# Kernel tuning notes

Measured on AMD Instinct MI355X. Metric: run time of the kernel, lower is better.

Reference implementation:

```python
import jax, jax.numpy as jnp
import numpy as np

EMBED_DIM = 512
NUM_HEADS = 8
HEAD_DIM = EMBED_DIM // NUM_HEADS
FFN_DIM = 4 * EMBED_DIM
B, S = 4, 2048
LN_EPS = 1e-5


def _linear_params(key, fan_in, fan_out):
    kw, kb = jax.random.split(key)
    bound = 1.0 / np.sqrt(fan_in)
    W = jax.random.uniform(kw, (fan_in, fan_out), jnp.float32, -bound, bound)
    b = jax.random.uniform(kb, (fan_out,), jnp.float32, -bound, bound)
    return W, b


def setup_inputs() -> dict:
    key = jax.random.key(0)
    ks = jax.random.split(key, 10)
    query = jax.random.normal(ks[0], (B, S, EMBED_DIM), jnp.float32)
    key_t = jax.random.normal(ks[1], (B, S, EMBED_DIM), jnp.float32)
    value = jax.random.normal(ks[2], (B, S, EMBED_DIM), jnp.float32)
    Wq, bq = _linear_params(ks[3], EMBED_DIM, EMBED_DIM)
    Wk, bk = _linear_params(ks[4], EMBED_DIM, EMBED_DIM)
    Wv, bv = _linear_params(ks[5], EMBED_DIM, EMBED_DIM)
    Wo, bo = _linear_params(ks[6], EMBED_DIM, EMBED_DIM)
    W1, b1 = _linear_params(ks[7], EMBED_DIM, FFN_DIM)
    W2, b2 = _linear_params(ks[8], FFN_DIM, EMBED_DIM)
    g1 = jnp.ones((EMBED_DIM,), jnp.float32); be1 = jnp.zeros((EMBED_DIM,), jnp.float32)
    g2 = jnp.ones((EMBED_DIM,), jnp.float32); be2 = jnp.zeros((EMBED_DIM,), jnp.float32)
    return dict(query=query, key=key_t, value=value,
                Wq=Wq, bq=bq, Wk=Wk, bk=bk, Wv=Wv, bv=bv, Wo=Wo, bo=bo,
                g1=g1, be1=be1, g2=g2, be2=be2,
                W1=W1, b1=b1, W2=W2, b2=b2)


def _layernorm(x, g, b):
    mu = jnp.mean(x, axis=-1, keepdims=True)
    var = jnp.mean(jnp.square(x - mu), axis=-1, keepdims=True)
    return (x - mu) * jax.lax.rsqrt(var + LN_EPS) * g + b


def reference(query, key, value, Wq, bq, Wk, bk, Wv, bv, Wo, bo,
              g1, be1, g2, be2, W1, b1, W2, b2):
    b_, s_ = query.shape[:2]
    # projections -> [B, H, S, Dh]
    Q = (query @ Wq + bq).reshape(b_, -1, NUM_HEADS, HEAD_DIM).transpose(0, 2, 1, 3)
    K = (key @ Wk + bk).reshape(b_, -1, NUM_HEADS, HEAD_DIM).transpose(0, 2, 1, 3)
    V = (value @ Wv + bv).reshape(b_, -1, NUM_HEADS, HEAD_DIM).transpose(0, 2, 1, 3)
    scores = jnp.einsum('bhqd,bhkd->bhqk', Q, K) / jnp.sqrt(jnp.float32(HEAD_DIM))
    attn = jax.nn.softmax(scores, axis=-1)  # dropout is eval-mode identity
    ctx = jnp.einsum('bhqk,bhkd->bhqd', attn, V)
    ctx = ctx.transpose(0, 2, 1, 3).reshape(b_, -1, EMBED_DIM)
    out = ctx @ Wo + bo
    out = _layernorm(query + out, g1, be1)
    ffn = jax.nn.gelu(out @ W1 + b1, approximate=False) @ W2 + b2
    return _layernorm(out + ffn, g2, be2)
```

## Files before the change

### kernel.cpp

```cpp
#include <hip/hip_runtime.h>
#include <hip/hip_bf16.h>
#include <math.h>

#define EMBED 512
#define NHEAD 8
#define HDIM 64
#define FFN 2048
#define BB 4
#define SS 2048
#define MROWS (BB*SS)
#define NB ((size_t)MROWS * EMBED)
#define LN_EPS 1e-5f
#define QSCALE 0.180336880111f

typedef __attribute__((ext_vector_type(8))) short short8;
typedef __attribute__((ext_vector_type(4))) float floatx4;

__device__ inline float bf2f(__hip_bfloat16 x) { return __bfloat162float(x); }
__device__ inline __hip_bfloat16 f2bf(float x) { return __float2bfloat16(x); }

__device__ inline float gelu_f(float x) {
    return 0.5f * x * (1.0f + erff(x * 0.70710678118654752f));
}

__device__ inline void async_copy16(const void* g, void* l) {
    __builtin_amdgcn_global_load_lds(
        (const __attribute__((address_space(1))) void*)g,
        (__attribute__((address_space(3))) void*)l, 16, 0, 0);
}

__device__ inline int sane_f(float v) {
    return (v == v) && (fabsf(v) > 0x1p-40f) && (fabsf(v) < 0x1p40f);
}

__global__ void detect_kernel(const void* __restrict__ q, int* __restrict__ flag) {
    const float* qf = (const float*)q;
    int lane = threadIdx.x;
    float v = qf[lane * 1024 + 7];
    bool ok = sane_f(v);
    unsigned long long m = __ballot(ok);
    if (lane == 0) *flag = (__popcll(m) >= 32) ? 1 : 0;
}

__global__ __launch_bounds__(256) void prep_kernel(
    const void* __restrict__ query, const void* __restrict__ keyi, const void* __restrict__ vali,
    const void* __restrict__ Wq, const void* __restrict__ Wk, const void* __restrict__ Wv,
    const void* __restrict__ Wo, const void* __restrict__ W1, const void* __restrict__ W2,
    const void* __restrict__ bq, const void* __restrict__ bk, const void* __restrict__ bv,
    const void* __restrict__ bo, const void* __restrict__ b1, const void* __restrict__ b2,
    const void* __restrict__ g1, const void* __restrict__ be1,
    const void* __restrict__ g2, const void* __restrict__ be2,
    __hip_bfloat16* __restrict__ qkvbf,
    __hip_bfloat16* __restrict__ Wcat,
    __hip_bfloat16* __restrict__ biasb)
{
    __shared__ __hip_bfloat16 L[64][65];
    const int f32 = sane_f(((const float*)query)[7]) + sane_f(((const float*)query)[1031]) +
                    sane_f(((const float*)query)[200003]) + sane_f(((const float*)query)[1000003]) >= 3;
    const int t = threadIdx.x;
    const int blk = blockIdx.x;

    if (blk < 6144) {
        size_t pos = ((size_t)blk * 256 + t) * 8;
        int sel = (int)(pos >> 22);
        size_t off = pos & (NB - 1);
        const void* src = sel == 0 ? query : sel == 1 ? keyi : vali;
        if (f32) {
            const float* s = (const float*)src + off;
            float4 f0 = *reinterpret_cast<const float4*>(s);
            float4 f1 = *reinterpret_cast<const float4*>(s + 4);
            alignas(16) __hip_bfloat16 h[8] = {
                f2bf(f0.x), f2bf(f0.y), f2bf(f0.z), f2bf(f0.w),
                f2bf(f1.x), f2bf(f1.y), f2bf(f1.z), f2bf(f1.w)};
            *reinterpret_cast<uint4*>(qkvbf + pos) = *reinterpret_cast<const uint4*>(h);
        } else {
            *reinterpret_cast<uint4*>(qkvbf + pos) =
                *reinterpret_cast<const uint4*>((const __hip_bfloat16*)src + off);
        }
        return;
    }

    const void* src; __hip_bfloat16* dst; int R, C, r0, c0;
    if (blk < 6400) {
        int b2i = blk - 6144; src = W1; dst = Wcat + 4 * 512 * 512;
        R = 512; C = 2048; r0 = (b2i >> 5) * 64; c0 = (b2i & 31) * 64;
    } else if (blk < 6656) {
        int b3 = blk - 6400; src = W2; dst = Wcat + 4 * 512 * 512 + 512 * 2048;
        R = 2048; C = 512; r0 = (b3 >> 3) * 64; c0 = (b3 & 7) * 64;
    } else if (blk < 6912) {
        int b4 = blk - 6656; int which = b4 >> 6; int tile = b4 & 63;
        src = which == 0 ? Wq : which == 1 ? Wk : which == 2 ? Wv : Wo;
        dst = Wcat + (size_t)which * 512 * 512;
        R = 512; C = 512; r0 = (tile >> 3) * 64; c0 = (tile & 7) * 64;
    } else {
        const void* srcs[10] = {bq, bk, bv, bo, b1, b2, g1, be1, g2, be2};
        const int offs[10] = {0, 512, 1024, 1536, 2048, 4096, 4608, 5120, 5632, 6144};
        const int lens[10] = {512, 512, 512, 512, 2048, 512, 512, 512, 512, 512};
        for (int a = 0; a < 10; ++a)
            for (int i = t; i < lens[a]; i += 256)
                biasb[offs[a] + i] = f32 ? f2bf(((const float*)srcs[a])[i])
                                         : ((const __hip_bfloat16*)srcs[a])[i];
        return;
    }
    for (int c = t; c < 4096; c += 256) {
        int lr = c >> 6, lc = c & 63;
        L[lr][lc] = f32 ? f2bf(((const float*)src)[(size_t)(r0 + lr) * C + c0 + lc])
                        : ((const __hip_bfloat16*)src)[(size_t)(r0 + lr) * C + c0 + lc];
    }
    __syncthreads();
    for (int c = t; c < 4096; c += 256) {
        int lr = c >> 6, lc = c & 63;
        dst[(size_t)(c0 + lr) * R + r0 + lc] = L[lc][lr];
    }
}

template<int ACT, int BIAS>
__global__ __launch_bounds__(256) void gemm_bt_lds_kernel(
    const __hip_bfloat16* __restrict__ A,
    const __hip_bfloat16* __restrict__ Bt,
    const __hip_bfloat16* __restrict__ bias,
    __hip_bfloat16* __restrict__ C,
    int M, int N, int K, int ksplit)
{
    const int bm = blockIdx.x * 128;
    const int bn = blockIdx.y * 128;
    int kbeg = 0, kend = K;
    if (BIAS == 0) {
        kbeg = blockIdx.z * ksplit;
        kend = kbeg + ksplit;
        C += (size_t)blockIdx.z * NB;
    }
    const int t = threadIdx.x;
    const int wave = t >> 6, lane = t & 63;
    const int wm = (wave >> 1) * 64, wn = (wave & 1) * 64;
    const int quad = lane >> 4, r = lane & 15;

    __shared__ alignas(16) __hip_bfloat16 As[2][128 * 32];
    __shared__ alignas(16) __hip_bfloat16 Bs[2][128 * 32];

    floatx4 acc[4][4];
    #pragma unroll
    for (int i = 0; i < 4; ++i)
        #pragma unroll
        for (int j = 0; j < 4; ++j)
            acc[i][j] = (floatx4){0.f, 0.f, 0.f, 0.f};

    const int c0 = wave * 128;

    for (int kt = kbeg; kt < kend; kt += 64) {
        #pragma unroll
        for (int h = 0; h < 2; ++h) {
            #pragma unroll
            for (int it = 0; it < 2; ++it) {
                int c = c0 + it * 64 + lane;
                int row = c >> 2, col = (c & 3) * 8;
                async_copy16(A + (size_t)(bm + row) * K + kt + h * 32 + col,
                             As[h] + (size_t)(c0 + it * 64) * 8);
                async_copy16(Bt + (size_t)(bn + row) * K + kt + h * 32 + col,
                             Bs[h] + (size_t)(c0 + it * 64) * 8);
            }
        }
        __syncthreads();
        #pragma unroll
        for (int h = 0; h < 2; ++h) {
            short8 af[4], bfr[4];
            #pragma unroll
            for (int i = 0; i < 4; ++i)
                af[i] = *reinterpret_cast<const short8*>(&As[h][(wm + i * 16 + r) * 32 + quad * 8]);
            #pragma unroll
            for (int j = 0; j < 4; ++j)
                bfr[j] = *reinterpret_cast<const short8*>(&Bs[h][(wn + j * 16 + r) * 32 + quad * 8]);
            #pragma unroll
            for (int i = 0; i < 4; ++i)
                #pragma unroll
                for (int j = 0; j < 4; ++j)
                    acc[i][j] = __builtin_amdgcn_mfma_f32_16x16x32_bf16(af[i], bfr[j], acc[i][j], 0, 0, 0);
        }
        __syncthreads();
    }

    #pragma unroll
    for (int j = 0; j < 4; ++j) {
        const int n = bn + wn + j * 16 + r;
        float bvv = BIAS ? bf2f(bias[n]) : 0.f;
        #pragma unroll
        for (int i = 0; i < 4; ++i) {
            #pragma unroll
            for (int v = 0; v < 4; ++v) {
                int m = bm + wm + i * 16 + quad * 4 + v;
                float x = acc[i][j][v] + bvv;
                if (ACT == 1) x = gelu_f(x);
                C[(size_t)m * N + n] = f2bf(x);
            }
        }
    }
}

__global__ __launch_bounds__(256) void gemm_qkv_fused_kernel(
    const __hip_bfloat16* __restrict__ Acat,
    const __hip_bfloat16* __restrict__ Wcat,
    const __hip_bfloat16* __restrict__ biascat,
    __hip_bfloat16* __restrict__ Ocat)
{
    const int sel = blockIdx.x >> 6;
    const __hip_bfloat16* A = Acat + (size_t)sel * NB;
    const __hip_bfloat16* Bt = Wcat + (size_t)sel * 512 * 512;
    const __hip_bfloat16* bias = biascat + sel * 512;
    __hip_bfloat16* C = Ocat + (size_t)sel * NB;

    const int bm = (blockIdx.x & 63) * 128;
    const int bn = blockIdx.y * 128;
    const int t = threadIdx.x;
    const int wave = t >> 6, lane = t & 63;
    const int wm = (wave >> 1) * 64, wn = (wave & 1) * 64;
    const int quad = lane >> 4, r = lane & 15;
    const int K = EMBED, N = EMBED;

    __shared__ alignas(16) __hip_bfloat16 As[2][128 * 32];
    __shared__ alignas(16) __hip_bfloat16 Bs[2][128 * 32];

    floatx4 acc[4][4];
    #pragma unroll
    for (int i = 0; i < 4; ++i)
        #pragma unroll
        for (int j = 0; j < 4; ++j)
            acc[i][j] = (floatx4){0.f, 0.f, 0.f, 0.f};

    const int c0 = wave * 128;

    for (int kt = 0; kt < K; kt += 64) {
        #pragma unroll
        for (int h = 0; h < 2; ++h) {
            #pragma unroll
            for (int it = 0; it < 2; ++it) {
                int c = c0 + it * 64 + lane;
                int row = c >> 2, col = (c & 3) * 8;
                async_copy16(A + (size_t)(bm + row) * K + kt + h * 32 + col,
                             As[h] + (size_t)(c0 + it * 64) * 8);
                async_copy16(Bt + (size_t)(bn + row) * K + kt + h * 32 + col,
                             Bs[h] + (size_t)(c0 + it * 64) * 8);
            }
        }
        __syncthreads();
        #pragma unroll
        for (int h = 0; h < 2; ++h) {
            short8 af[4], bfr[4];
            #pragma unroll
            for (int i = 0; i < 4; ++i)
                af[i] = *reinterpret_cast<const short8*>(&As[h][(wm + i * 16 + r) * 32 + quad * 8]);
            #pragma unroll
            for (int j = 0; j < 4; ++j)
                bfr[j] = *reinterpret_cast<const short8*>(&Bs[h][(wn + j * 16 + r) * 32 + quad * 8]);
            #pragma unroll
            for (int i = 0; i < 4; ++i)
                #pragma unroll
                for (int j = 0; j < 4; ++j)
                    acc[i][j] = __builtin_amdgcn_mfma_f32_16x16x32_bf16(af[i], bfr[j], acc[i][j], 0, 0, 0);
        }
        __syncthreads();
    }

    #pragma unroll
    for (int j = 0; j < 4; ++j) {
        const int n = bn + wn + j * 16 + r;
        const float bvv = bf2f(bias[n]);
        #pragma unroll
        for (int i = 0; i < 4; ++i) {
            #pragma unroll
            for (int v = 0; v < 4; ++v) {
                int m = bm + wm + i * 16 + quad * 4 + v;
                C[(size_t)m * N + n] = f2bf(acc[i][j][v] + bvv);
            }
        }
    }
}

__global__ __launch_bounds__(256) void vtrans_kernel(
    const __hip_bfloat16* __restrict__ Vb, __hip_bfloat16* __restrict__ Vt)
{
    const int bh = blockIdx.y;
    const int b = bh >> 3, h = bh & 7;
    const int s0 = blockIdx.x * 64;
    __shared__ alignas(16) __hip_bfloat16 L[64][72];
    const int t = threadIdx.x;
    for (int c = t; c < 512; c += 256) {
        int row = c >> 3, g = c & 7;
        *reinterpret_cast<uint4*>(&L[row][g * 8]) =
            *reinterpret_cast<const uint4*>(Vb + (size_t)(b * SS + s0 + row) * EMBED + h * 64 + g * 8);
    }
    __syncthreads();
    for (int c = t; c < 512; c += 256) {
        int d = c >> 3, g = c & 7;
        alignas(16) __hip_bfloat16 tmp[8];
        #pragma unroll
        for (int j = 0; j < 8; ++j) tmp[j] = L[g * 8 + j][d];
        *reinterpret_cast<uint4*>(Vt + ((size_t)bh * 64 + d) * SS + s0 + g * 8) =
            *reinterpret_cast<const uint4*>(tmp);
    }
}

__global__ __launch_bounds__(256) void attn_mfma_kernel(
    const __hip_bfloat16* __restrict__ Qg,
    const __hip_bfloat16* __restrict__ Kg,
    const __hip_bfloat16* __restrict__ Vt,
    __hip_bfloat16* __restrict__ Apart0,
    __hip_bfloat16* __restrict__ Apart1,
    float* __restrict__ lbuf)
{
    const int bh = blockIdx.y;
    const int b = bh >> 3, h = bh & 7;
    const int q0 = blockIdx.x * 128;
    const int z = blockIdx.z;
    const int t = threadIdx.x;
    const int w = t >> 6, lane = t & 63;
    const int quad = lane >> 4, r = lane & 15;

    __shared__ alignas(16) __hip_bfloat16 Ks[2][64 * 32];
    __shared__ alignas(16) __hip_bfloat16 Vs[2][64 * 32];
    __shared__ alignas(16) __hip_bfloat16 Ps[4][32][72];

    const size_t bbase = (size_t)b * SS * EMBED;
    const size_t hoff = (size_t)h * HDIM;
    const size_t vtbase = (size_t)bh * HDIM * SS;

    short8 aq[2][2];
    #pragma unroll
    for (int s = 0; s < 2; ++s) {
        const __hip_bfloat16* qrow = Qg + bbase + (size_t)(q0 + w * 32 + s * 16 + r) * EMBED + hoff;
        short8 t0 = *reinterpret_cast<const short8*>(qrow + quad * 8);
        short8 t1 = *reinterpret_cast<const short8*>(qrow + 32 + quad * 8);
        #pragma unroll
        for (int i = 0; i < 8; ++i) {
            ((__hip_bfloat16*)&aq[s][0])[i] = f2bf(bf2f(((const __hip_bfloat16*)&t0)[i]) * QSCALE);
            ((__hip_bfloat16*)&aq[s][1])[i] = f2bf(bf2f(((const __hip_bfloat16*)&t1)[i]) * QSCALE);
        }
    }

    const short one = 0x3F80;
    const short8 bones = {one, one, one, one, one, one, one, one};

    const int tensor = w >> 1, slab = w & 1;
    const int srow = lane >> 2;
    const int scol = (((lane & 3) ^ ((srow >> 1) & 3)) * 8);
    const int cs = ((r >> 1) & 3) * 8;

    floatx4 o0[4], o1[4], l0a, l1a;
    #pragma unroll
    for (int nt = 0; nt < 4; ++nt) {
        o0[nt] = (floatx4){0.f, 0.f, 0.f, 0.f};
        o1[nt] = (floatx4){0.f, 0.f, 0.f, 0.f};
    }
    l0a = (floatx4){0.f, 0.f, 0.f, 0.f};
    l1a = (floatx4){0.f, 0.f, 0.f, 0.f};

    const int kbeg = z * (SS / 2), kend = kbeg + SS / 2;
    const __hip_bfloat16* kp[4];
    const __hip_bfloat16* vp[4];
    #pragma unroll
    for (int g = 0; g < 4; ++g) {
        int row = g * 16 + srow;
        kp[g] = Kg + bbase + (size_t)(kbeg + row) * EMBED + hoff + slab * 32 + scol;
        vp[g] = Vt + vtbase + (size_t)row * SS + kbeg + slab * 32 + scol;
    }

    for (int kt = kbeg; kt < kend; kt += 64) {
        __syncthreads();
        if (tensor == 0) {
            #pragma unroll
            for (int g = 0; g < 4; ++g) {
                async_copy16(kp[g], &Ks[slab][g * 512]);
                kp[g] += 64 * EMBED;
            }
        } else {
            #pragma unroll
            for (int g = 0; g < 4; ++g) {
                async_copy16(vp[g], &Vs[slab][g * 512]);
                vp[g] += 64;
            }
        }
        __syncthreads();

        floatx4 s0[4], s1[4];
        #pragma unroll
        for (int nt = 0; nt < 4; ++nt) {
            s0[nt] = (floatx4){0.f, 0.f, 0.f, 0.f};
            s1[nt] = (floatx4){0.f, 0.f, 0.f, 0.f};
        }
        #pragma unroll
        for (int nt = 0; nt < 4; ++nt) {
            short8 ak0 = *reinterpret_cast<const short8*>(&Ks[0][(nt * 16 + r) * 32 + (quad * 8 ^ cs)]);
            short8 ak1 = *reinterpret_cast<const short8*>(&Ks[1][(nt * 16 + r) * 32 + (quad * 8 ^ cs)]);
            s0[nt] = __builtin_amdgcn_mfma_f32_16x16x32_bf16(ak0, aq[0][0], s0[nt], 0, 0, 0);
            s0[nt] = __builtin_amdgcn_mfma_f32_16x16x32_bf16(ak1, aq[0][1], s0[nt], 0, 0, 0);
            s1[nt] = __builtin_amdgcn_mfma_f32_16x16x32_bf16(ak0, aq[1][0], s1[nt], 0, 0, 0);
            s1[nt] = __builtin_amdgcn_mfma_f32_16x16x32_bf16(ak1, aq[1][1], s1[nt], 0, 0, 0);
        }

        #pragma unroll
        for (int s = 0; s < 2; ++s) {
            floatx4* sc = s == 0 ? s0 : s1;
            #pragma unroll
            for (int nt = 0; nt < 4; ++nt) {
                float p0 = exp2f(sc[nt][0]), p1 = exp2f(sc[nt][1]);
                float p2 = exp2f(sc[nt][2]), p3 = exp2f(sc[nt][3]);
                __hip_bfloat162 pa = __float22bfloat162_rn(make_float2(p0, p1));
                __hip_bfloat162 pb = __float22bfloat162_rn(make_float2(p2, p3));
                uint2 u;
                u.x = *reinterpret_cast<unsigned*>(&pa);
                u.y = *reinterpret_cast<unsigned*>(&pb);
                *reinterpret_cast<uint2*>(&Ps[w][s * 16 + r][nt * 16 + quad * 4]) = u;
            }
        }

        short8 ap00 = *reinterpret_cast<const short8*>(&Ps[w][r][quad * 8]);
        short8 ap01 = *reinterpret_cast<const short8*>(&Ps[w][r][32 + quad * 8]);
        short8 ap10 = *reinterpret_cast<const short8*>(&Ps[w][16 + r][quad * 8]);
        short8 ap11 = *reinterpret_cast<const short8*>(&Ps[w][16 + r][32 + quad * 8]);
        #pragma unroll
        for (int nt = 0; nt < 4; ++nt) {
            short8 bv0 = *reinterpret_cast<const short8*>(&Vs[0][(nt * 16 + r) * 32 + (quad * 8 ^ cs)]);
            short8 bv1 = *reinterpret_cast<const short8*>(&Vs[1][(nt * 16 + r) * 32 + (quad * 8 ^ cs)]);
            o0[nt] = __builtin_amdgcn_mfma_f32_16x16x32_bf16(ap00, bv0, o0[nt], 0, 0, 0);
            o0[nt] = __builtin_amdgcn_mfma_f32_16x16x32_bf16(ap01, bv1, o0[nt], 0, 0, 0);
            o1[nt] = __builtin_amdgcn_mfma_f32_16x16x32_bf16(ap10, bv0, o1[nt], 0, 0, 0);
            o1[nt] = __builtin_amdgcn_mfma_f32_16x16x32_bf16(ap11, bv1, o1[nt], 0, 0, 0);
        }
        l0a = __builtin_amdgcn_mfma_f32_16x16x32_bf16(ap00, bones, l0a, 0, 0, 0);
        l0a = __builtin_amdgcn_mfma_f32_16x16x32_bf16(ap01, bones, l0a, 0, 0, 0);
        l1a = __builtin_amdgcn_mfma_f32_16x16x32_bf16(ap10, bones, l1a, 0, 0, 0);
        l1a = __builtin_amdgcn_mfma_f32_16x16x32_bf16(ap11, bones, l1a, 0, 0, 0);
    }

    __hip_bfloat16* Ap = z == 0 ? Apart0 : Apart1;
    #pragma unroll
    for (int s = 0; s < 2; ++s) {
        floatx4* oa = s == 0 ? o0 : o1;
        floatx4 la = s == 0 ? l0a : l1a;
        #pragma unroll
        for (int v = 0; v < 4; ++v) {
            int q = q0 + w * 32 + s * 16 + quad * 4 + v;
            __hip_bfloat16* orow = Ap + bbase + (size_t)q * EMBED + hoff;
            #pragma unroll
            for (int nt = 0; nt < 4; ++nt)
                orow[nt * 16 + r] = f2bf(oa[nt][v]);
            if (r == 0)
                lbuf[((size_t)z * 32 + bh) * SS + q] = la[v];
        }
    }
}

__global__ __launch_bounds__(256) void attn_combine_kernel(
    const __hip_bfloat16* __restrict__ Apart0,
    const __hip_bfloat16* __restrict__ Apart1,
    const float* __restrict__ lbuf,
    __hip_bfloat16* __restrict__ ctx)
{
    const int bh = blockIdx.y;
    const int b = bh >> 3, h = bh & 7;
    const int q0 = blockIdx.x * 64;
    const int t = threadIdx.x;
    __shared__ float winv[64];

    if (t < 64) {
        float l0 = lbuf[(size_t)bh * SS + q0 + t];
        float l1 = lbuf[((size_t)32 + bh) * SS + q0 + t];
        winv[t] = 1.0f / (l0 + l1);
    }
    __syncthreads();

    const size_t base = (size_t)b * SS * EMBED + (size_t)h * HDIM;
    for (int c = t; c < 512; c += 256) {
        int q = c >> 3, d8 = (c & 7) * 8;
        size_t off = base + (size_t)(q0 + q) * EMBED + d8;
        short8 a0v = *reinterpret_cast<const short8*>(Apart0 + off);
        short8 a1v = *reinterpret_cast<const short8*>(Apart1 + off);
        float si = winv[q];
        alignas(16) __hip_bfloat16 o[8];
        #pragma unroll
        for (int j = 0; j < 8; ++j) {
            float x0 = bf2f(((const __hip_bfloat16*)&a0v)[j]);
            float x1 = bf2f(((const __hip_bfloat16*)&a1v)[j]);
            o[j] = f2bf((x0 + x1) * si);
        }
        *reinterpret_cast<uint4*>(ctx + off) = *reinterpret_cast<const uint4*>(o);
    }
}

template<int OUT32>
__global__ __launch_bounds__(256) void add_ln_split_kernel(
    const __hip_bfloat16* __restrict__ X,
    const __hip_bfloat16* __restrict__ Y0,
    const __hip_bfloat16* __restrict__ Y1,
    const __hip_bfloat16* __restrict__ bias,
    const __hip_bfloat16* __restrict__ g,
    const __hip_bfloat16* __restrict__ bt,
    void* __restrict__ out,
    const int* __restrict__ dflag)
{
    const int w = threadIdx.x >> 6, lane = threadIdx.x & 63;
    const int row = blockIdx.x * 4 + w;
    const size_t base = (size_t)row * EMBED + lane * 8;
    const int co = lane * 8;

    short8 xv  = *reinterpret_cast<const short8*>(X + base);
    short8 y0v = *reinterpret_cast<const short8*>(Y0 + base);
    short8 y1v = *reinterpret_cast<const short8*>(Y1 + base);
    short8 bv  = *reinterpret_cast<const short8*>(bias + co);

    float x[8];
    float s = 0.f;
    #pragma unroll
    for (int j = 0; j < 8; ++j) {
        x[j] = bf2f(((const __hip_bfloat16*)&xv)[j]) + bf2f(((const __hip_bfloat16*)&y0v)[j])
             + bf2f(((const __hip_bfloat16*)&y1v)[j]) + bf2f(((const __hip_bfloat16*)&bv)[j]);
        s += x[j];
    }
    #pragma unroll
    for (int off = 32; off; off >>= 1) s += __shfl_xor(s, off, 64);
    const float mu = s * (1.0f / EMBED);
    float vs = 0.f;
    #pragma unroll
    for (int j = 0; j < 8; ++j) { x[j] -= mu; vs += x[j] * x[j]; }
    #pragma unroll
    for (int off = 32; off; off >>= 1) vs += __shfl_xor(vs, off, 64);
    const float rstd = rsqrtf(vs * (1.0f / EMBED) + LN_EPS);

    short8 gv  = *reinterpret_cast<const short8*>(g + co);
    short8 btv = *reinterpret_cast<const short8*>(bt + co);
    if (OUT32 && *dflag) {
        float4 o0, o1;
        float of[8];
        #pragma unroll
        for (int j = 0; j < 8; ++j)
            of[j] = x[j] * rstd * bf2f(((const __hip_bfloat16*)&gv)[j]) + bf2f(((const __hip_bfloat16*)&btv)[j]);
        o0 = make_float4(of[0], of[1], of[2], of[3]);
        o1 = make_float4(of[4], of[5], of[6], of[7]);
        *reinterpret_cast<float4*>((float*)out + base) = o0;
        *reinterpret_cast<float4*>((float*)out + base + 4) = o1;
    } else {
        alignas(16) __hip_bfloat16 o[8];
        #pragma unroll
        for (int j = 0; j < 8; ++j)
            o[j] = f2bf(x[j] * rstd * bf2f(((const __hip_bfloat16*)&gv)[j]) + bf2f(((const __hip_bfloat16*)&btv)[j]));
        *reinterpret_cast<uint4*>((__hip_bfloat16*)out + base) = *reinterpret_cast<const uint4*>(o);
    }
}

extern "C" void kernel_launch(void* const* d_in, const int* in_sizes, int n_in,
                              void* d_out, int out_size, void* d_ws, size_t ws_size,
                              hipStream_t stream)
{
    (void)in_sizes; (void)n_in; (void)out_size; (void)ws_size;

    const void* query = d_in[0];
    const void* keyi  = d_in[1];
    const void* vali  = d_in[2];
    const void* Wq = d_in[3];  const void* bq = d_in[4];
    const void* Wk = d_in[5];  const void* bk = d_in[6];
    const void* Wv = d_in[7];  const void* bv = d_in[8];
    const void* Wo = d_in[9];  const void* bo = d_in[10];
    const void* g1 = d_in[11]; const void* be1 = d_in[12];
    const void* g2 = d_in[13]; const void* be2 = d_in[14];
    const void* W1 = d_in[15]; const void* b1 = d_in[16];
    const void* W2 = d_in[17]; const void* b2 = d_in[18];

    int* dflag = (int*)d_ws;
    __hip_bfloat16* biasb = (__hip_bfloat16*)((char*)d_ws + 64);
    __hip_bfloat16* Wcat = biasb + 8192;
    __hip_bfloat16* buf = Wcat + 4 * 512 * 512 + 2 * 512 * 2048;
    __hip_bfloat16* bqkvb = biasb;
    __hip_bfloat16* bob  = biasb + 1536;
    __hip_bfloat16* b1b  = biasb + 2048;
    __hip_bfloat16* b2b  = biasb + 4096;
    __hip_bfloat16* g1b  = biasb + 4608;
    __hip_bfloat16* be1b = biasb + 5120;
    __hip_bfloat16* g2b  = biasb + 5632;
    __hip_bfloat16* be2b = biasb + 6144;
    __hip_bfloat16* qkvbf  = buf;
    __hip_bfloat16* QKVo   = buf + 3 * NB;
    __hip_bfloat16* Qb = QKVo;
    __hip_bfloat16* Kb = QKVo + NB;
    __hip_bfloat16* Vb = QKVo + 2 * NB;
    __hip_bfloat16* Vt     = buf + 1 * NB;
    __hip_bfloat16* Apart0 = buf + 2 * NB;
    __hip_bfloat16* Apart1 = buf + 6 * NB;
    float*          lbuf   = (float*)(buf + 7 * NB);
    __hip_bfloat16* ctx    = buf + 3 * NB;
    __hip_bfloat16* Yw     = buf + 4 * NB;
    __hip_bfloat16* x1     = buf + 3 * NB;
    __hip_bfloat16* hbf    = buf + 4 * NB;
    __hip_bfloat16* Yf     = buf + 1 * NB;

    detect_kernel<<<1, 64, 0, stream>>>(query, dflag);

    prep_kernel<<<6913, 256, 0, stream>>>(
        query, keyi, vali, Wq, Wk, Wv, Wo, W1, W2,
        bq, bk, bv, bo, b1, b2, g1, be1, g2, be2,
        qkvbf, Wcat, biasb);

    gemm_qkv_fused_kernel<<<dim3(192, 4), 256, 0, stream>>>(qkvbf, Wcat, bqkvb, QKVo);

    vtrans_kernel<<<dim3(SS / 64, BB * NHEAD), 256, 0, stream>>>(Vb, Vt);

    attn_mfma_kernel<<<dim3(SS / 128, BB * NHEAD, 2), 256, 0, stream>>>(
        Qb, Kb, Vt, Apart0, Apart1, lbuf);
    attn_combine_kernel<<<dim3(SS / 64, BB * NHEAD), 256, 0, stream>>>(
        Apart0, Apart1, lbuf, ctx);

    gemm_bt_lds_kernel<0, 0><<<dim3(MROWS / 128, EMBED / 128, 2), 256, 0, stream>>>(
        ctx, Wcat + 3 * 512 * 512, nullptr, Yw, MROWS, EMBED, EMBED, EMBED / 2);
    add_ln_split_kernel<0><<<MROWS / 4, 256, 0, stream>>>(
        qkvbf, Yw, Yw + NB, bob, g1b, be1b, x1, dflag);

    gemm_bt_lds_kernel<1, 1><<<dim3(MROWS / 128, FFN / 128), 256, 0, stream>>>(
        x1, Wcat + 4 * 512 * 512, b1b, hbf, MROWS, FFN, EMBED, 0);
    gemm_bt_lds_kernel<0, 0><<<dim3(MROWS / 128, EMBED / 128, 2), 256, 0, stream>>>(
        hbf, Wcat + 4 * 512 * 512 + 512 * 2048, nullptr, Yf, MROWS, EMBED, FFN, FFN / 2);
    add_ln_split_kernel<1><<<MROWS / 4, 256, 0, stream>>>(
        x1, Yf, Yf + NB, b2b, g2b, be2b, d_out, dflag);
}
```

Before: 331.7 us.

## Double-buffer K/V tiles in attention kernel and raise MFMA wave priority

The attention kernel now keeps two LDS buffers for the K and V tiles. It issues the async copy of the next 64-key tile before computing on the current one, and uses a single barrier per iteration instead of two. This is meant to hide global-to-LDS load latency behind the QK and PV MFMA work. s_setprio is also raised around the MFMA blocks so those waves get scheduling preference. LDS per block roughly doubles for K/V, which may reduce the number of resident blocks per CU.

```diff
diff --git a/kernel.cpp b/kernel.cpp
--- a/kernel.cpp
+++ b/kernel.cpp
@@ -315,8 +315,8 @@
     const int w = t >> 6, lane = t & 63;
     const int quad = lane >> 4, r = lane & 15;
 
-    __shared__ alignas(16) __hip_bfloat16 Ks[2][64 * 32];
-    __shared__ alignas(16) __hip_bfloat16 Vs[2][64 * 32];
+    __shared__ alignas(16) __hip_bfloat16 Ks[2][2][64 * 32];
+    __shared__ alignas(16) __hip_bfloat16 Vs[2][2][64 * 32];
     __shared__ alignas(16) __hip_bfloat16 Ps[4][32][72];
 
     const size_t bbase = (size_t)b * SS * EMBED;
@@ -363,22 +363,38 @@
         vp[g] = Vt + vtbase + (size_t)row * SS + kbeg + slab * 32 + scol;
     }
 
+    if (tensor == 0) {
+        #pragma unroll
+        for (int g = 0; g < 4; ++g) {
+            async_copy16(kp[g], &Ks[0][slab][g * 512]);
+            kp[g] += 64 * EMBED;
+        }
+    } else {
+        #pragma unroll
+        for (int g = 0; g < 4; ++g) {
+            async_copy16(vp[g], &Vs[0][slab][g * 512]);
+            vp[g] += 64;
+        }
+    }
+    __syncthreads();
+
+    int cur = 0;
     for (int kt = kbeg; kt < kend; kt += 64) {
-        __syncthreads();
-        if (tensor == 0) {
-            #pragma unroll
-            for (int g = 0; g < 4; ++g) {
-                async_copy16(kp[g], &Ks[slab][g * 512]);
-                kp[g] += 64 * EMBED;
+        if (kt + 64 < kend) {
+            if (tensor == 0) {
+                #pragma unroll
+                for (int g = 0; g < 4; ++g) {
+                    async_copy16(kp[g], &Ks[cur ^ 1][slab][g * 512]);
+                    kp[g] += 64 * EMBED;
+                }
+            } else {
+                #pragma unroll
+                for (int g = 0; g < 4; ++g) {
+                    async_copy16(vp[g], &Vs[cur ^ 1][slab][g * 512]);
+                    vp[g] += 64;
+                }
             }
-        } else {
-            #pragma unroll
-            for (int g = 0; g < 4; ++g) {
-                async_copy16(vp[g], &Vs[slab][g * 512]);
-                vp[g] += 64;
-            }
-        }
-        __syncthreads();
+        }
 
         floatx4 s0[4], s1[4];
         #pragma unroll
@@ -386,15 +402,17 @@
             s0[nt] = (floatx4){0.f, 0.f, 0.f, 0.f};
             s1[nt] = (floatx4){0.f, 0.f, 0.f, 0.f};
         }
+        __builtin_amdgcn_s_setprio(1);
         #pragma unroll
         for (int nt = 0; nt < 4; ++nt) {
-            short8 ak0 = *reinterpret_cast<const short8*>(&Ks[0][(nt * 16 + r) * 32 + (quad * 8 ^ cs)]);
-            short8 ak1 = *reinterpret_cast<const short8*>(&Ks[1][(nt * 16 + r) * 32 + (quad * 8 ^ cs)]);
+            short8 ak0 = *reinterpret_cast<const short8*>(&Ks[cur][0][(nt * 16 + r) * 32 + (quad * 8 ^ cs)]);
+            short8 ak1 = *reinterpret_cast<const short8*>(&Ks[cur][1][(nt * 16 + r) * 32 + (quad * 8 ^ cs)]);
             s0[nt] = __builtin_amdgcn_mfma_f32_16x16x32_bf16(ak0, aq[0][0], s0[nt], 0, 0, 0);
             s0[nt] = __builtin_amdgcn_mfma_f32_16x16x32_bf16(ak1, aq[0][1], s0[nt], 0, 0, 0);
             s1[nt] = __builtin_amdgcn_mfma_f32_16x16x32_bf16(ak0, aq[1][0], s1[nt], 0, 0, 0);
             s1[nt] = __builtin_amdgcn_mfma_f32_16x16x32_bf16(ak1, aq[1][1], s1[nt], 0, 0, 0);
         }
+        __builtin_amdgcn_s_setprio(0);
 
         #pragma unroll
         for (int s = 0; s < 2; ++s) {
@@ -416,10 +434,11 @@
         short8 ap01 = *reinterpret_cast<const short8*>(&Ps[w][r][32 + quad * 8]);
         short8 ap10 = *reinterpret_cast<const short8*>(&Ps[w][16 + r][quad * 8]);
         short8 ap11 = *reinterpret_cast<const short8*>(&Ps[w][16 + r][32 + quad * 8]);
+        __builtin_amdgcn_s_setprio(1);
         #pragma unroll
         for (int nt = 0; nt < 4; ++nt) {
-            short8 bv0 = *reinterpret_cast<const short8*>(&Vs[0][(nt * 16 + r) * 32 + (quad * 8 ^ cs)]);
-            short8 bv1 = *reinterpret_cast<const short8*>(&Vs[1][(nt * 16 + r) * 32 + (quad * 8 ^ cs)]);
+            short8 bv0 = *reinterpret_cast<const short8*>(&Vs[cur][0][(nt * 16 + r) * 32 + (quad * 8 ^ cs)]);
+            short8 bv1 = *reinterpret_cast<const short8*>(&Vs[cur][1][(nt * 16 + r) * 32 + (quad * 8 ^ cs)]);
             o0[nt] = __builtin_amdgcn_mfma_f32_16x16x32_bf16(ap00, bv0, o0[nt], 0, 0, 0);
             o0[nt] = __builtin_amdgcn_mfma_f32_16x16x32_bf16(ap01, bv1, o0[nt], 0, 0, 0);
             o1[nt] = __builtin_amdgcn_mfma_f32_16x16x32_bf16(ap10, bv0, o1[nt], 0, 0, 0);
@@ -429,6 +448,10 @@
         l0a = __builtin_amdgcn_mfma_f32_16x16x32_bf16(ap01, bones, l0a, 0, 0, 0);
         l1a = __builtin_amdgcn_mfma_f32_16x16x32_bf16(ap10, bones, l1a, 0, 0, 0);
         l1a = __builtin_amdgcn_mfma_f32_16x16x32_bf16(ap11, bones, l1a, 0, 0, 0);
+        __builtin_amdgcn_s_setprio(0);
+
+        __syncthreads();
+        cur ^= 1;
     }
 
     __hip_bfloat16* Ap = z == 0 ? Apart0 : Apart1;
```

Measured after the change: 332.6 us. No clear change (+0.3%).
